# Kernel optimization log

Hardware: AMD Instinct MI355X
Metric: run time of the kernel (lower is better)

## Reference

```python
import jax, jax.numpy as jnp
import numpy as np

N_NODES = 50000
N_EDGES = 800000
IN_CH = 128
OUT_CH = 128


def setup_inputs() -> dict:
    key = jax.random.key(0)
    k1, k2, k3 = jax.random.split(key, 3)
    x = jax.random.normal(k1, (N_NODES, IN_CH), dtype=jnp.float32)
    edge_index = jax.random.randint(k2, (2, N_EDGES), 0, N_NODES, dtype=jnp.int32)
    # GCNConv weight (glorot-ish) and bias
    W = jax.random.normal(k3, (IN_CH, OUT_CH), dtype=jnp.float32) / np.sqrt(IN_CH)
    b = jnp.zeros((OUT_CH,), dtype=jnp.float32)
    return {"x": x, "edge_index": edge_index, "W": W, "b": b}


def reference(x, edge_index, W, b):
    # FairGCNAutoEncoder.forward == encode: GCNConv(x, edge_index) -> ReLU
    n = x.shape[0]
    src, dst = edge_index[0], edge_index[1]
    # PyG GCNConv default: add self-loops with weight 1
    loops = jnp.arange(n, dtype=edge_index.dtype)
    src = jnp.concatenate([src, loops])
    dst = jnp.concatenate([dst, loops])
    # linear transform first (standard GCNConv: lin has no bias; bias added post-agg)
    h = x @ W  # [N, out]
    # symmetric normalization deg^{-1/2}[src] * deg^{-1/2}[dst], deg from dst (col)
    deg = jax.ops.segment_sum(jnp.ones((src.shape[0],), dtype=h.dtype), dst,
                              num_segments=n)
    dinv = jax.lax.rsqrt(jnp.where(deg > 0, deg, 1.0))
    norm = dinv[src] * dinv[dst]  # [E+N]
    msgs = h[src] * norm[:, None]  # gather + scale, [E+N, out]
    agg = jax.ops.segment_sum(msgs, dst, num_segments=n)  # scatter-add
    return jax.nn.relu(agg + b)
```

## Files before the change

### kernel.cpp

```cpp
#include <hip/hip_runtime.h>

#define CH 128
#define GM 64
#define LDK 136
#define BSH 5
#define BNODES 32
#define CAP 768
#define MAXB 2048
#define EPB 8192

typedef _Float16 f16x4 __attribute__((ext_vector_type(4)));
typedef float    f32x4 __attribute__((ext_vector_type(4)));
typedef unsigned short u16x8 __attribute__((ext_vector_type(8)));

static __host__ __device__ inline size_t align256(size_t x) { return (x + 255) & ~(size_t)255; }

__device__ inline unsigned short f2b(float f) {
    unsigned int u = __float_as_uint(f);
    return (unsigned short)((u + 0x7fffu + ((u >> 16) & 1u)) >> 16);
}
__device__ inline float b2f(unsigned short h) {
    return __uint_as_float(((unsigned int)h) << 16);
}


__global__ __launch_bounds__(256) void k_bin(const int* __restrict__ ei,
                                             int* __restrict__ gcur,
                                             unsigned int* __restrict__ pairs,
                                             unsigned int* __restrict__ spill,
                                             int e, int nb,
                                             const float* __restrict__ W,
                                             unsigned short* __restrict__ WT) {
    __shared__ int lcnt[MAXB], lbase[MAXB], lpos[MAXB];
    const int t = threadIdx.x;

    if (blockIdx.x < 8) {
        int wb = blockIdx.x * 2048;
#pragma unroll
        for (int i = 0; i < 8; ++i) {
            int idx = wb + t + i * 256;
            int k = idx >> 7, nn = idx & 127;
            _Float16 h = (_Float16)W[idx];
            WT[nn * CH + k] = *(unsigned short*)&h;
        }
    }

    for (int i = t; i < nb; i += 256) { lcnt[i] = 0; lpos[i] = 0; }
    __syncthreads();

    const int base = blockIdx.x * EPB;
    const int e4 = e >> 2;
    int4 s4[8], d4[8];
#pragma unroll
    for (int r = 0; r < 8; ++r) {
        int q = (base >> 2) + t + r * 256;
        if (q < e4) {
            s4[r] = ((const int4*)ei)[q];
            d4[r] = ((const int4*)(ei + e))[q];
        } else {
            s4[r] = make_int4(-1, -1, -1, -1);
            d4[r] = make_int4(0, 0, 0, 0);
        }
    }
    const int* ss = (const int*)s4;
    const int* dd = (const int*)d4;
#pragma unroll
    for (int i = 0; i < 32; ++i)
        if (ss[i] >= 0) atomicAdd(&lcnt[dd[i] >> BSH], 1);
    __syncthreads();
    for (int i = t; i < nb; i += 256)
        if (lcnt[i]) lbase[i] = atomicAdd(&gcur[i], lcnt[i]);
    __syncthreads();
#pragma unroll
    for (int i = 0; i < 32; ++i) {
        if (ss[i] >= 0) {
            int b = dd[i] >> BSH;
            int p = lbase[b] + atomicAdd(&lpos[b], 1);
            if (p < CAP) {
                pairs[(size_t)b * CAP + p] = ((unsigned)ss[i] << BSH) | (unsigned)(dd[i] & (BNODES - 1));
            } else {
                int sp = atomicAdd(&gcur[nb], 1);
                spill[sp] = ((unsigned)ss[i] << 16) | (unsigned)dd[i];
            }
        }
    }
}


__global__ __launch_bounds__(256) void k_gemm(const float* __restrict__ x,
                                              const unsigned short* __restrict__ WT,
                                              const unsigned int* __restrict__ pairs,
                                              const int* __restrict__ gcur,
                                              const unsigned int* __restrict__ spill,
                                              float* __restrict__ dinv,
                                              unsigned short* __restrict__ hs_b,
                                              int n, int nb) {
    __shared__ unsigned short sA[GM * LDK];
    __shared__ unsigned short sB[CH * LDK];
    __shared__ int   scnt[GM];
    __shared__ float sdv[GM];

    const int tid = threadIdx.x;
    const int b   = blockIdx.x;
    const int r0  = b * GM;

    if (tid < GM) scnt[tid] = 0;

    const u16x8* Wv = (const u16x8*)WT;
#pragma unroll
    for (int i = 0; i < 8; ++i) {
        int c = tid + i * 256;
        int nr = c >> 4, kq = c & 15;
        *(u16x8*)&sB[nr * LDK + kq * 8] = Wv[c];
    }
#pragma unroll
    for (int i = 0; i < 8; ++i) {
        int c = tid + i * 256;
        int r = c >> 5, cq = c & 31;
        float4 v = make_float4(0.f, 0.f, 0.f, 0.f);
        if (r0 + r < n) v = ((const float4*)x)[(size_t)(r0 + r) * 32 + cq];
        f16x4 h;
        h[0] = (_Float16)v.x; h[1] = (_Float16)v.y;
        h[2] = (_Float16)v.z; h[3] = (_Float16)v.w;
        *(f16x4*)&sA[r * LDK + cq * 4] = h;
    }
    __syncthreads();

    {
#pragma unroll
        for (int q = 0; q < 2; ++q) {
            const int bk = 2 * b + q;
            if (bk < nb) {
                const int cntb = min(gcur[bk], CAP);
                const unsigned int* pp = pairs + (size_t)bk * CAP;
                for (int j = tid; j < cntb; j += 256)
                    atomicAdd(&scnt[q * BNODES + (pp[j] & (BNODES - 1))], 1);
            }
        }
        const int ns = gcur[nb];
        if (ns > 0) {
            for (int j = tid; j < ns; j += 256) {
                unsigned u = spill[j];
                unsigned du = u & 0xffffu;
                if ((int)(du >> 6) == b) atomicAdd(&scnt[du & 63], 1);
            }
        }
    }

    const int lane = tid & 63, w = tid >> 6;
    const int mh = (w >> 1) * 32;
    const int nh = (w & 1) * 64;
    const int fr = lane & 15, fg = lane >> 4;

    f32x4 acc[2][4];
#pragma unroll
    for (int a = 0; a < 2; ++a)
#pragma unroll
        for (int bq = 0; bq < 4; ++bq) acc[a][bq] = (f32x4){0.f, 0.f, 0.f, 0.f};

#pragma unroll
    for (int ks = 0; ks < 8; ++ks) {
        const int kk = ks * 16 + fg * 4;
        f16x4 a0 = *(const f16x4*)&sA[(mh + fr) * LDK + kk];
        f16x4 a1 = *(const f16x4*)&sA[(mh + 16 + fr) * LDK + kk];
        f16x4 b0 = *(const f16x4*)&sB[(nh + fr) * LDK + kk];
        f16x4 b1 = *(const f16x4*)&sB[(nh + 16 + fr) * LDK + kk];
        f16x4 b2 = *(const f16x4*)&sB[(nh + 32 + fr) * LDK + kk];
        f16x4 b3 = *(const f16x4*)&sB[(nh + 48 + fr) * LDK + kk];
        acc[0][0] = __builtin_amdgcn_mfma_f32_16x16x16f16(a0, b0, acc[0][0], 0, 0, 0);
        acc[0][1] = __builtin_amdgcn_mfma_f32_16x16x16f16(a0, b1, acc[0][1], 0, 0, 0);
        acc[0][2] = __builtin_amdgcn_mfma_f32_16x16x16f16(a0, b2, acc[0][2], 0, 0, 0);
        acc[0][3] = __builtin_amdgcn_mfma_f32_16x16x16f16(a0, b3, acc[0][3], 0, 0, 0);
        acc[1][0] = __builtin_amdgcn_mfma_f32_16x16x16f16(a1, b0, acc[1][0], 0, 0, 0);
        acc[1][1] = __builtin_amdgcn_mfma_f32_16x16x16f16(a1, b1, acc[1][1], 0, 0, 0);
        acc[1][2] = __builtin_amdgcn_mfma_f32_16x16x16f16(a1, b2, acc[1][2], 0, 0, 0);
        acc[1][3] = __builtin_amdgcn_mfma_f32_16x16x16f16(a1, b3, acc[1][3], 0, 0, 0);
    }
    __syncthreads();

    if (tid < GM) {
        float dv = rsqrtf((float)scnt[tid] + 1.0f);
        sdv[tid] = dv;
        int node = r0 + tid;
        if (node < n) dinv[node] = dv;
    }
    __syncthreads();

#pragma unroll
    for (int mt = 0; mt < 2; ++mt) {
        int lbase_r = mh + mt * 16 + fg * 4;
        int rbase = r0 + lbase_r;
#pragma unroll
        for (int nt = 0; nt < 4; ++nt) {
            int col = nh + nt * 16 + fr;
#pragma unroll
            for (int rg = 0; rg < 4; ++rg) {
                if (rbase + rg < n)
                    hs_b[(size_t)(rbase + rg) * CH + col] = f2b(acc[mt][nt][rg] * sdv[lbase_r + rg]);
            }
        }
    }
}


__global__ __launch_bounds__(256) void k_gagg(const u16x8* __restrict__ h8,
                                              const unsigned int* __restrict__ pairs,
                                              const int* __restrict__ gcur,
                                              const unsigned int* __restrict__ spill,
                                              const float* __restrict__ dinv,
                                              const float* __restrict__ bias,
                                              float* __restrict__ out, int n, int nb) {
    __shared__ unsigned int   sPairs[CAP];
    __shared__ unsigned short sSort[CAP];
    __shared__ int scnt[BNODES], sexcl[BNODES], scur[BNODES];
    __shared__ float sdinv[BNODES];

    const int t = threadIdx.x, b = blockIdx.x;
    const int n0 = b * BNODES;

    if (t < BNODES) {
        scnt[t] = 0;
        int node = n0 + t;
        sdinv[t] = (node < n) ? dinv[node] : 0.f;
    }
    __syncthreads();

    const int cntb = min(gcur[b], CAP);
    const unsigned int* pp = pairs + (size_t)b * CAP;
    for (int j = t; j < cntb; j += 256) {
        unsigned p = pp[j];
        sPairs[j] = p;
        atomicAdd(&scnt[p & (BNODES - 1)], 1);
    }
    __syncthreads();

    if (t < 32) {
        int c = scnt[t];
        int s = c;
#pragma unroll
        for (int off = 1; off < 32; off <<= 1) {
            int tv = __shfl_up(s, off, 64);
            if (t >= off) s += tv;
        }
        sexcl[t] = s - c;
        scur[t]  = s - c;
    }
    __syncthreads();

    for (int j = t; j < cntb; j += 256) {
        unsigned p = sPairs[j];
        int pos = atomicAdd(&scur[p & (BNODES - 1)], 1);
        sSort[pos] = (unsigned short)(p >> BSH);
    }
    __syncthreads();

    const int g = t >> 4, lane = t & 15;
    const int ns = gcur[nb];
#pragma unroll
    for (int k = 0; k < BNODES / 16; ++k) {
        const int nl = g * (BNODES / 16) + k;
        const int node = n0 + nl;
        if (node >= n) break;

        float acc[8];
        {
            u16x8 v = h8[(size_t)node * 16 + lane];
#pragma unroll
            for (int i = 0; i < 8; ++i) acc[i] = b2f(v[i]);
        }

        int j = sexcl[nl];
        const int end = j + scnt[nl];
        for (; j + 4 <= end; j += 4) {
            int s0 = sSort[j + 0], s1 = sSort[j + 1];
            int s2 = sSort[j + 2], s3 = sSort[j + 3];
            u16x8 v0 = h8[(size_t)s0 * 16 + lane];
            u16x8 v1 = h8[(size_t)s1 * 16 + lane];
            u16x8 v2 = h8[(size_t)s2 * 16 + lane];
            u16x8 v3 = h8[(size_t)s3 * 16 + lane];
#pragma unroll
            for (int i = 0; i < 8; ++i)
                acc[i] += (b2f(v0[i]) + b2f(v1[i])) + (b2f(v2[i]) + b2f(v3[i]));
        }
        for (; j < end; ++j) {
            u16x8 v = h8[(size_t)sSort[j] * 16 + lane];
#pragma unroll
            for (int i = 0; i < 8; ++i) acc[i] += b2f(v[i]);
        }

        if (ns > 0) {
            for (int q = 0; q < ns; ++q) {
                unsigned u = spill[q];
                if ((int)(u & 0xffffu) == node) {
                    u16x8 v = h8[(size_t)(u >> 16) * 16 + lane];
#pragma unroll
                    for (int i = 0; i < 8; ++i) acc[i] += b2f(v[i]);
                }
            }
        }

        const float di = sdinv[nl];
        const float* bp = bias + lane * 8;
        float4 o0, o1;
        o0.x = fmaxf(fmaf(acc[0], di, bp[0]), 0.f);
        o0.y = fmaxf(fmaf(acc[1], di, bp[1]), 0.f);
        o0.z = fmaxf(fmaf(acc[2], di, bp[2]), 0.f);
        o0.w = fmaxf(fmaf(acc[3], di, bp[3]), 0.f);
        o1.x = fmaxf(fmaf(acc[4], di, bp[4]), 0.f);
        o1.y = fmaxf(fmaf(acc[5], di, bp[5]), 0.f);
        o1.z = fmaxf(fmaf(acc[6], di, bp[6]), 0.f);
        o1.w = fmaxf(fmaf(acc[7], di, bp[7]), 0.f);
        float4* op = (float4*)(out + (size_t)node * CH + lane * 8);
        op[0] = o0;
        op[1] = o1;
    }
}


extern "C" void kernel_launch(void* const* d_in, const int* in_sizes, int n_in,
                              void* d_out, int out_size, void* d_ws, size_t ws_size,
                              hipStream_t stream) {
    const float* x  = (const float*)d_in[0];
    const int*   ei = (const int*)d_in[1];
    const float* W  = (const float*)d_in[2];
    const float* b  = (const float*)d_in[3];
    float* out = (float*)d_out;

    const int N = in_sizes[0] / CH;
    const int E = in_sizes[1] / 2;

    const int NB = (N + BNODES - 1) / BNODES;
    const int GB = (N + GM - 1) / GM;

    size_t o_gcur  = 0;
    size_t o_dinv  = o_gcur  + align256(((size_t)NB + 1) * 4);
    size_t o_WT    = o_dinv  + align256((size_t)N * 4);
    size_t o_hs    = o_WT    + align256((size_t)CH * CH * 2);
    size_t o_pairs = o_hs    + align256((size_t)N * CH * 2);
    size_t o_spill = o_pairs + align256((size_t)NB * CAP * 4);

    int*            gcur  = (int*)((char*)d_ws + o_gcur);
    float*          dinv  = (float*)((char*)d_ws + o_dinv);
    unsigned short* WT    = (unsigned short*)((char*)d_ws + o_WT);
    unsigned short* hs_b  = (unsigned short*)((char*)d_ws + o_hs);
    unsigned int*   pairs = (unsigned int*)((char*)d_ws + o_pairs);
    unsigned int*   spill = (unsigned int*)((char*)d_ws + o_spill);

    const int gCH = (E + EPB - 1) / EPB;

    hipMemsetAsync(gcur, 0, ((size_t)NB + 1) * 4, stream);
    k_bin<<<gCH, 256, 0, stream>>>(ei, gcur, pairs, spill, E, NB, W, WT);
    k_gemm<<<GB, 256, 0, stream>>>(x, WT, pairs, gcur, spill, dinv, hs_b, N, NB);
    k_gagg<<<NB, 256, 0, stream>>>((const u16x8*)hs_b, pairs, gcur, spill, dinv, b, out, N, NB);
}
```

Baseline: 74.48 us.

## Split gathered features into XCD-pinned column planes for L2 locality

```diff
diff --git a/kernel.cpp b/kernel.cpp
--- a/kernel.cpp
+++ b/kernel.cpp
@@ -8,6 +8,7 @@
 #define CAP 768
 #define MAXB 2048
 #define EPB 8192
+#define SLICES 4
 
 typedef _Float16 f16x4 __attribute__((ext_vector_type(4)));
 typedef float    f32x4 __attribute__((ext_vector_type(4)));
@@ -193,17 +194,19 @@
 #pragma unroll
         for (int nt = 0; nt < 4; ++nt) {
             int col = nh + nt * 16 + fr;
+            int pl = col >> 5, cs = col & 31;
+            unsigned short* plane = hs_b + (size_t)pl * n * 32;
 #pragma unroll
             for (int rg = 0; rg < 4; ++rg) {
                 if (rbase + rg < n)
-                    hs_b[(size_t)(rbase + rg) * CH + col] = f2b(acc[mt][nt][rg] * sdv[lbase_r + rg]);
-            }
-        }
-    }
-}
-
-
-__global__ __launch_bounds__(256) void k_gagg(const u16x8* __restrict__ h8,
+                    plane[(size_t)(rbase + rg) * 32 + cs] = f2b(acc[mt][nt][rg] * sdv[lbase_r + rg]);
+            }
+        }
+    }
+}
+
+
+__global__ __launch_bounds__(256) void k_gagg(const unsigned short* __restrict__ hs_b,
                                               const unsigned int* __restrict__ pairs,
                                               const int* __restrict__ gcur,
                                               const unsigned int* __restrict__ spill,
@@ -215,7 +218,11 @@
     __shared__ int scnt[BNODES], sexcl[BNODES], scur[BNODES];
     __shared__ float sdinv[BNODES];
 
-    const int t = threadIdx.x, b = blockIdx.x;
+    const int t = threadIdx.x;
+    const int xcd = blockIdx.x & 7;
+    const int s   = xcd >> 1;
+    const int b   = (blockIdx.x >> 3) * 2 + (xcd & 1);
+    if (b >= nb) return;
     const int n0 = b * BNODES;
 
     if (t < BNODES) {
@@ -236,14 +243,14 @@
 
     if (t < 32) {
         int c = scnt[t];
-        int s = c;
+        int sc = c;
 #pragma unroll
         for (int off = 1; off < 32; off <<= 1) {
-            int tv = __shfl_up(s, off, 64);
-            if (t >= off) s += tv;
-        }
-        sexcl[t] = s - c;
-        scur[t]  = s - c;
+            int tv = __shfl_up(sc, off, 64);
+            if (t >= off) sc += tv;
+        }
+        sexcl[t] = sc - c;
+        scur[t]  = sc - c;
     }
     __syncthreads();
 
@@ -254,6 +261,7 @@
     }
     __syncthreads();
 
+    const unsigned short* plane = hs_b + (size_t)s * n * 32;
     const int g = t >> 4, lane = t & 15;
     const int ns = gcur[nb];
 #pragma unroll
@@ -262,11 +270,11 @@
         const int node = n0 + nl;
         if (node >= n) break;
 
-        float acc[8];
+        float a0, a1;
         {
-            u16x8 v = h8[(size_t)node * 16 + lane];
-#pragma unroll
-            for (int i = 0; i < 8; ++i) acc[i] = b2f(v[i]);
+            unsigned v = *(const unsigned*)&plane[(size_t)node * 32 + lane * 2];
+            a0 = b2f((unsigned short)v);
+            a1 = b2f((unsigned short)(v >> 16));
         }
 
         int j = sexcl[nl];
@@ -274,45 +282,38 @@
         for (; j + 4 <= end; j += 4) {
             int s0 = sSort[j + 0], s1 = sSort[j + 1];
             int s2 = sSort[j + 2], s3 = sSort[j + 3];
-            u16x8 v0 = h8[(size_t)s0 * 16 + lane];
-            u16x8 v1 = h8[(size_t)s1 * 16 + lane];
-            u16x8 v2 = h8[(size_t)s2 * 16 + lane];
-            u16x8 v3 = h8[(size_t)s3 * 16 + lane];
-#pragma unroll
-            for (int i = 0; i < 8; ++i)
-                acc[i] += (b2f(v0[i]) + b2f(v1[i])) + (b2f(v2[i]) + b2f(v3[i]));
+            unsigned v0 = *(const unsigned*)&plane[(size_t)s0 * 32 + lane * 2];
+            unsigned v1 = *(const unsigned*)&plane[(size_t)s1 * 32 + lane * 2];
+            unsigned v2 = *(const unsigned*)&plane[(size_t)s2 * 32 + lane * 2];
+            unsigned v3 = *(const unsigned*)&plane[(size_t)s3 * 32 + lane * 2];
+            a0 += (b2f((unsigned short)v0) + b2f((unsigned short)v1))
+                + (b2f((unsigned short)v2) + b2f((unsigned short)v3));
+            a1 += (b2f((unsigned short)(v0 >> 16)) + b2f((unsigned short)(v1 >> 16)))
+                + (b2f((unsigned short)(v2 >> 16)) + b2f((unsigned short)(v3 >> 16)));
         }
         for (; j < end; ++j) {
-            u16x8 v = h8[(size_t)sSort[j] * 16 + lane];
-#pragma unroll
-            for (int i = 0; i < 8; ++i) acc[i] += b2f(v[i]);
+            unsigned v = *(const unsigned*)&plane[(size_t)sSort[j] * 32 + lane * 2];
+            a0 += b2f((unsigned short)v);
+            a1 += b2f((unsigned short)(v >> 16));
         }
 
         if (ns > 0) {
             for (int q = 0; q < ns; ++q) {
                 unsigned u = spill[q];
                 if ((int)(u & 0xffffu) == node) {
-                    u16x8 v = h8[(size_t)(u >> 16) * 16 + lane];
-#pragma unroll
-                    for (int i = 0; i < 8; ++i) acc[i] += b2f(v[i]);
+                    unsigned v = *(const unsigned*)&plane[(size_t)(u >> 16) * 32 + lane * 2];
+                    a0 += b2f((unsigned short)v);
+                    a1 += b2f((unsigned short)(v >> 16));
                 }
             }
         }
 
         const float di = sdinv[nl];
-        const float* bp = bias + lane * 8;
-        float4 o0, o1;
-        o0.x = fmaxf(fmaf(acc[0], di, bp[0]), 0.f);
-        o0.y = fmaxf(fmaf(acc[1], di, bp[1]), 0.f);
-        o0.z = fmaxf(fmaf(acc[2], di, bp[2]), 0.f);
-        o0.w = fmaxf(fmaf(acc[3], di, bp[3]), 0.f);
-        o1.x = fmaxf(fmaf(acc[4], di, bp[4]), 0.f);
-        o1.y = fmaxf(fmaf(acc[5], di, bp[5]), 0.f);
-        o1.z = fmaxf(fmaf(acc[6], di, bp[6]), 0.f);
-        o1.w = fmaxf(fmaf(acc[7], di, bp[7]), 0.f);
-        float4* op = (float4*)(out + (size_t)node * CH + lane * 8);
-        op[0] = o0;
-        op[1] = o1;
+        const int col = s * 32 + lane * 2;
+        float2 o;
+        o.x = fmaxf(fmaf(a0, di, bias[col]), 0.f);
+        o.y = fmaxf(fmaf(a1, di, bias[col + 1]), 0.f);
+        *(float2*)(out + (size_t)node * CH + col) = o;
     }
 }
 
@@ -347,9 +348,10 @@
     unsigned int*   spill = (unsigned int*)((char*)d_ws + o_spill);
 
     const int gCH = (E + EPB - 1) / EPB;
+    const int gAG = ((NB + 1) / 2) * 8;
 
     hipMemsetAsync(gcur, 0, ((size_t)NB + 1) * 4, stream);
     k_bin<<<gCH, 256, 0, stream>>>(ei, gcur, pairs, spill, E, NB, W, WT);
     k_gemm<<<GB, 256, 0, stream>>>(x, WT, pairs, gcur, spill, dinv, hs_b, N, NB);
-    k_gagg<<<NB, 256, 0, stream>>>((const u16x8*)hs_b, pairs, gcur, spill, dinv, b, out, N, NB);
-}
+    k_gagg<<<gAG, 256, 0, stream>>>(hs_b, pairs, gcur, spill, dinv, b, out, N, NB);
+}
```

Result: slower. 78.97 us (+6.0%).
